# Performance work log

Measured on AMD Instinct MI355X. Metric: run time of the kernel, lower is better.

The kernel has to match this reference:

```python
import jax, jax.numpy as jnp
import numpy as np

B, S = 256, 200
VOCAB, E, H, OUT = 1002, 512, 512, 500
USERS, SKILLS = 50000, 500
PAD = 0


def setup_inputs() -> dict:
    key = jax.random.key(0)
    ks = jax.random.split(key, 16)
    s = 1.0 / np.sqrt(H)
    inp = {
        'input': jax.random.randint(ks[0], (B, S), 0, VOCAB),
        'target_id': jax.random.randint(ks[1], (B, 1), 0, OUT),
        'user_id_sequence': jax.random.randint(ks[2], (B, S), 0, USERS),
        'skill_sequence': jax.random.randint(ks[3], (B, S), 0, SKILLS),
        'attempt_sequence': jax.random.randint(ks[4], (B, S), 0, 100),
        # embeddings (padding_idx=0 -> zero row, as in torch)
        'enc_emb': (jax.random.normal(ks[5], (VOCAB, E)) * 0.02).at[PAD].set(0.0),
        'user_emb': (jax.random.normal(ks[6], (USERS, SKILLS)) * 0.02).at[PAD].set(0.0),
        'skill_emb': (jax.random.normal(ks[7], (SKILLS, SKILLS)) * 0.02).at[PAD].set(0.0),
        # MF.linear1: 2*skill_num -> hidden_dim
        'mf_W': jax.random.normal(ks[8], (H, 2 * SKILLS)) * 0.02,
        'mf_b': jnp.zeros((H,)),
        # LSTMCell params (torch gate order: i, f, g, o)
        'W_ih': jax.random.uniform(ks[9], (4 * H, E), minval=-s, maxval=s),
        'W_hh': jax.random.uniform(ks[10], (4 * H, H), minval=-s, maxval=s),
        'b_ih': jax.random.uniform(ks[11], (4 * H,), minval=-s, maxval=s),
        'b_hh': jax.random.uniform(ks[12], (4 * H,), minval=-s, maxval=s),
        # decoder: hidden -> output_dim
        'dec_W': jax.random.normal(ks[13], (OUT, H)) * 0.02,
        'dec_b': jnp.zeros((OUT,)),
    }
    return inp


def reference(input, target_id, user_id_sequence, skill_sequence, attempt_sequence,
              enc_emb, user_emb, skill_emb, mf_W, mf_b,
              W_ih, W_hh, b_ih, b_hh, dec_W, dec_b):
    # encoder embedding: (B, S, E)
    x = enc_emb[input]
    # MF branch: concat user/skill embeddings -> linear -> (B, S, H)
    ev = jnp.concatenate([user_emb[user_id_sequence], skill_emb[skill_sequence]], axis=-1)
    ext = jnp.einsum('bsf,hf->bsh', ev, mf_W) + mf_b

    def step(carry, ts):
        ht, ct = carry
        xt, et = ts  # (B, E), (B, H)
        ht = ht * jax.nn.sigmoid(et)  # custom per-step gating
        gates = xt @ W_ih.T + b_ih + ht @ W_hh.T + b_hh  # (B, 4H)
        i, f, g, o = jnp.split(gates, 4, axis=-1)
        ct = jax.nn.sigmoid(f) * ct + jax.nn.sigmoid(i) * jnp.tanh(g)
        ht = jax.nn.sigmoid(o) * jnp.tanh(ct)
        return (ht, ct), None

    h0 = jnp.zeros((B, H), dtype=x.dtype)
    (ht, _), _ = jax.lax.scan(step, (h0, h0),
                              (x.transpose(1, 0, 2), ext.transpose(1, 0, 2)))
    out = ht @ dec_W.T + dec_b  # (B, OUT)
    out = jnp.take_along_axis(out, target_id, axis=-1)  # (B, 1)
    return jax.nn.sigmoid(out)
```

## Files before the change

### kernel.cpp

```cpp
#include <hip/hip_runtime.h>
#include <stdint.h>

typedef __bf16 bf16x8 __attribute__((ext_vector_type(8)));
typedef float f32x4 __attribute__((ext_vector_type(4)));

#define MFMA16(a, b, c) __builtin_amdgcn_mfma_f32_16x16x32_bf16((a), (b), (c), 0, 0, 0)

__device__ __forceinline__ float sigf(float x) { return 1.f / (1.f + __expf(-x)); }
__device__ __forceinline__ float tanhfast(float x) { return 1.f - 2.f / (__expf(2.f * x) + 1.f); }
__device__ __forceinline__ float bf2f(uint16_t u) {
  union { float f; uint32_t i; } v; v.i = ((uint32_t)u) << 16; return v.f;
}
__device__ __forceinline__ uint16_t f2bf(float f) {
  union { float f; uint32_t i; } v; v.f = f;
  return (uint16_t)((v.i + 0x7FFFu + ((v.i >> 16) & 1u)) >> 16);
}
__device__ __forceinline__ bf16x8 cvt8(const float* __restrict__ p) {
  f32x4 a = *(const f32x4*)p;
  f32x4 b = *(const f32x4*)(p + 4);
  bf16x8 r;
  r[0] = (__bf16)a[0]; r[1] = (__bf16)a[1]; r[2] = (__bf16)a[2]; r[3] = (__bf16)a[3];
  r[4] = (__bf16)b[0]; r[5] = (__bf16)b[1]; r[6] = (__bf16)b[2]; r[7] = (__bf16)b[3];
  return r;
}

__global__ __launch_bounds__(256) void k_prep(
    const float* __restrict__ mf_W, uint16_t* __restrict__ mfWb) {
  const int idx = blockIdx.x * 256 + threadIdx.x;
  const int h = idx >> 10, k = idx & 1023;
  const float v = (k < 1000) ? mf_W[(size_t)h * 1000 + k] : 0.f;
  mfWb[idx] = f2bf(v);
}

__global__ __launch_bounds__(256) void k_encW(
    const float* __restrict__ enc_emb,
    const float* __restrict__ W_ih,
    const float* __restrict__ b_ih,
    const float* __restrict__ b_hh,
    uint16_t* __restrict__ encWb)
{
  const int w = threadIdx.x >> 6, l = threadIdx.x & 63;
  const int mblk = blockIdx.x & 15;
  const int nblk = blockIdx.x >> 4;
  const int kg = l >> 4;
  const int arow = mblk * 64 + w * 16 + (l & 15);
  const bool rowok = arow < 1002;

  f32x4 acc[4] = {};
  for (int kk = 0; kk < 16; ++kk) {
    const int kc = kk * 32 + kg * 8;
    bf16x8 a = {};
    if (rowok) a = cvt8(enc_emb + (size_t)arow * 512 + kc);
#pragma unroll
    for (int n = 0; n < 4; ++n) {
      const int wrow = nblk * 64 + n * 16 + (l & 15);
      bf16x8 b = cvt8(W_ih + (size_t)wrow * 512 + kc);
      acc[n] = MFMA16(a, b, acc[n]);
    }
  }
  const int orow = mblk * 64 + w * 16 + kg * 4;
#pragma unroll
  for (int n = 0; n < 4; ++n) {
    const int col = nblk * 64 + n * 16 + (l & 15);
    const float bias = b_ih[col] + b_hh[col];
#pragma unroll
    for (int j = 0; j < 4; ++j) {
      const int rrow = orow + j;
      if (rrow < 1002) encWb[(size_t)rrow * 2048 + col] = f2bf(acc[n][j] + bias);
    }
  }
}

__global__ __launch_bounds__(256, 2) void k_fused(
    const int* __restrict__ inp,
    const float* __restrict__ W_hh,
    const uint16_t* __restrict__ encWb,
    const int* __restrict__ uid, const int* __restrict__ sid,
    const float* __restrict__ user_emb,
    const float* __restrict__ skill_emb,
    const uint16_t* __restrict__ mfWb,
    const float* __restrict__ mf_b,
    uint16_t* __restrict__ ext,
    uint16_t* __restrict__ hbuf,
    float* __restrict__ hfinal,
    uint32_t* __restrict__ extCnt)
{
  __shared__ __align__(1024) char ldsbuf[65536];

  const int tid = threadIdx.x;
  const int w = tid >> 6, l = tid & 63, kg = l >> 4;

  if (blockIdx.x >= 256) {
    char* As = ldsbuf;
    const int bx = blockIdx.x - 256;
    const int s  = bx >> 2;
    const int bq = bx & 3;

    const int srow = tid >> 2;
    const int q = tid & 3;
    const int m = (bq * 64 + srow) * 200 + s;
    const float* up = user_emb + (size_t)uid[m] * 500;
    const float* sp = skill_emb + (size_t)sid[m] * 500;

    f32x4 acc[4][8] = {};

#pragma unroll
    for (int ks = 0; ks < 2; ++ks) {
      if (ks) __syncthreads();
#pragma unroll
      for (int j = 0; j < 16; ++j) {
        const int e0 = ks * 512 + q * 128 + j * 8;
        bf16x8 av = {};
        if (e0 + 8 <= 500) {
          av = cvt8(up + e0);
        } else if (e0 == 496) {
          f32x4 a4 = *(const f32x4*)(up + 496);
          f32x4 b4 = *(const f32x4*)sp;
          av[0] = (__bf16)a4[0]; av[1] = (__bf16)a4[1]; av[2] = (__bf16)a4[2]; av[3] = (__bf16)a4[3];
          av[4] = (__bf16)b4[0]; av[5] = (__bf16)b4[1]; av[6] = (__bf16)b4[2]; av[7] = (__bf16)b4[3];
        } else if (e0 + 8 <= 1000) {
          av = cvt8(sp + (e0 - 500));
        }
        const int kb = (q * 128 + j * 8) * 2;
        *(bf16x8*)(As + srow * 1024 + (kb ^ ((srow & 7) << 4))) = av;
      }
      __syncthreads();

      for (int kk = 0; kk < 16; ++kk) {
        bf16x8 a[4];
#pragma unroll
        for (int rf = 0; rf < 4; ++rf) {
          const int row = rf * 16 + (l & 15);
          a[rf] = *(const bf16x8*)(As + row * 1024 +
                                   ((kk * 64 + kg * 16) ^ ((row & 7) << 4)));
        }
#pragma unroll
        for (int n = 0; n < 8; ++n) {
          const int col = w * 128 + n * 16 + (l & 15);
          bf16x8 b = *(const bf16x8*)(mfWb + (size_t)col * 1024 + ks * 512 + kk * 32 + kg * 8);
#pragma unroll
          for (int rf = 0; rf < 4; ++rf)
            acc[rf][n] = MFMA16(a[rf], b, acc[rf][n]);
        }
      }
    }

#pragma unroll
    for (int rf = 0; rf < 4; ++rf)
#pragma unroll
      for (int n = 0; n < 8; ++n) {
        const int col = w * 128 + n * 16 + (l & 15);
        const float bias = mf_b[col];
#pragma unroll
        for (int j = 0; j < 4; ++j) {
          const int bl = rf * 16 + kg * 4 + j;
          const size_t grow = (size_t)(bq * 64 + bl) * 200 + s;
          ext[grow * 512 + col] = f2bf(acc[rf][n][j] + bias);
        }
      }
    asm volatile("s_waitcnt vmcnt(0)" ::: "memory");
    __syncthreads();
    if (tid == 0) {
      asm volatile("buffer_wbl2 sc1\n\ts_waitcnt vmcnt(0)" ::: "memory");
      __hip_atomic_fetch_add(extCnt + s * 16, 1u, __ATOMIC_RELAXED, __HIP_MEMORY_SCOPE_AGENT);
    }
    return;
  }

  uint16_t* htgS        = (uint16_t*)ldsbuf;
  float (*gbuf)[16][32] = (float(*)[16][32])(ldsbuf + 16384);
  float (*ctS)[32]      = (float(*)[32])(ldsbuf + 24576);
  int (*inpS)[200]      = (int(*)[200])(ldsbuf + 26624);

  const int c = blockIdx.x & 15;
  const int r = blockIdx.x >> 4;
  const int row0 = r * 16;

  bf16x8 wfrag[16][2];
#pragma unroll
  for (int kk = 0; kk < 16; ++kk) {
#pragma unroll
    for (int n = 0; n < 2; ++n) {
      const int wrow = w * 512 + c * 32 + n * 16 + (l & 15);
      wfrag[kk][n] = cvt8(W_hh + (size_t)wrow * 512 + kk * 32 + kg * 8);
    }
  }
  for (int e = tid; e < 512; e += 256) ctS[e >> 5][e & 31] = 0.f;
  for (int e = tid; e < 2048; e += 256) ((uint64_t*)htgS)[e] = 0ull;
  for (int e = tid; e < 16 * 200; e += 256)
    inpS[e / 200][e % 200] = inp[(row0 + e / 200) * 200 + (e % 200)];

  const int grow_ = l >> 2;
  const int gch = l & 3;
  const int urr = tid >> 4;
  const int uh2 = (tid & 15) << 1;
  const int ub = row0 + urr;

  __syncthreads();

  f32x4 acc[2];
#pragma unroll
  for (int n = 0; n < 2; ++n)
#pragma unroll
    for (int j = 0; j < 4; ++j) {
      const int col = w * 512 + c * 32 + n * 16 + (l & 15);
      acc[n][j] = bf2f(encWb[(size_t)inpS[kg * 4 + j][0] * 2048 + col]);
    }
  while (__hip_atomic_load(extCnt + 16, __ATOMIC_RELAXED, __HIP_MEMORY_SCOPE_AGENT) < 4u)
    __builtin_amdgcn_s_sleep(1);
  uint32_t ep = __hip_atomic_load(
      (const uint32_t*)(ext + (size_t)ub * 200 * 512 + 512 + c * 32 + uh2),
      __ATOMIC_RELAXED, __HIP_MEMORY_SCOPE_AGENT);

  for (int t = 0; t < 200; ++t) {
    if (t > 0) {
      const uint32_t tag = (uint32_t)((t >> 1) & 3);
      const uint64_t pat64 = ((uint64_t)((tag & 1u) | ((tag >> 1) << 16))) * 0x0000000100000001ull;
      const uint16_t* hb = hbuf + (size_t)(t & 1) * (256 * 512);
      const uint64_t* sp[4];
      uint64_t v[4][2];
#pragma unroll
      for (int p = 0; p < 4; ++p) {
        sp[p] = (const uint64_t*)(hb + (size_t)(row0 + grow_) * 512 + (w * 4 + p) * 32 + gch * 8);
        v[p][0] = __hip_atomic_load(sp[p],     __ATOMIC_RELAXED, __HIP_MEMORY_SCOPE_AGENT);
        v[p][1] = __hip_atomic_load(sp[p] + 1, __ATOMIC_RELAXED, __HIP_MEMORY_SCOPE_AGENT);
      }
#pragma unroll
      for (int p = 0; p < 4; ++p) {
        while ((v[p][0] & 0x0001000100010001ull) != pat64 ||
               (v[p][1] & 0x0001000100010001ull) != pat64) {
          __builtin_amdgcn_s_sleep(1);
          v[p][0] = __hip_atomic_load(sp[p],     __ATOMIC_RELAXED, __HIP_MEMORY_SCOPE_AGENT);
          v[p][1] = __hip_atomic_load(sp[p] + 1, __ATOMIC_RELAXED, __HIP_MEMORY_SCOPE_AGENT);
        }
      }
#pragma unroll
      for (int p = 0; p < 4; ++p) {
        const int prod = w * 4 + p;
        const int baddr = grow_ * 1024 + (((prod * 64) + gch * 16) ^ ((grow_ & 7) << 4));
        *(uint64_t*)((char*)htgS + baddr)     = v[p][0];
        *(uint64_t*)((char*)htgS + baddr + 8) = v[p][1];
      }
    }
    __syncthreads();

    const int ar = l & 15;
#pragma unroll
    for (int kk = 0; kk < 16; ++kk) {
      bf16x8 a = *(const bf16x8*)((char*)htgS + ar * 1024 +
                                  ((kk * 64 + kg * 16) ^ ((ar & 7) << 4)));
      acc[0] = MFMA16(a, wfrag[kk][0], acc[0]);
      acc[1] = MFMA16(a, wfrag[kk][1], acc[1]);
    }
#pragma unroll
    for (int n = 0; n < 2; ++n)
#pragma unroll
      for (int j = 0; j < 4; ++j)
        gbuf[w][kg * 4 + j][n * 16 + (l & 15)] = acc[n][j];
    __syncthreads();

    {
      float hv[2];
#pragma unroll
      for (int p = 0; p < 2; ++p) {
        const int h = uh2 + p;
        const float ig = sigf(gbuf[0][urr][h]);
        const float fg = sigf(gbuf[1][urr][h]);
        const float gg = tanhfast(gbuf[2][urr][h]);
        const float og = sigf(gbuf[3][urr][h]);
        const float cv = fg * ctS[urr][h] + ig * gg;
        ctS[urr][h] = cv;
        hv[p] = og * tanhfast(cv);
      }
      if (t < 199) {
        const float g0 = sigf(bf2f((uint16_t)(ep & 0xFFFFu)));
        const float g1 = sigf(bf2f((uint16_t)(ep >> 16)));
        const uint32_t tagn = (uint32_t)(((t + 1) >> 1) & 3);
        const uint32_t tpat = (tagn & 1u) | ((tagn >> 1) << 16);
        uint32_t pk = (uint32_t)f2bf(hv[0] * g0) | ((uint32_t)f2bf(hv[1] * g1) << 16);
        pk = (pk & ~0x00010001u) | tpat;
        uint32_t* hw = (uint32_t*)(hbuf + (size_t)((t + 1) & 1) * (256 * 512) +
                                   (size_t)ub * 512 + c * 32 + uh2);
        __hip_atomic_store(hw, pk, __ATOMIC_RELAXED, __HIP_MEMORY_SCOPE_AGENT);
      } else {
        hfinal[(size_t)ub * 512 + c * 32 + uh2]     = hv[0];
        hfinal[(size_t)ub * 512 + c * 32 + uh2 + 1] = hv[1];
      }
    }

    if (t < 199) {
      const int tn = t + 1;
#pragma unroll
      for (int n = 0; n < 2; ++n)
#pragma unroll
        for (int j = 0; j < 4; ++j) {
          const int col = w * 512 + c * 32 + n * 16 + (l & 15);
          acc[n][j] = bf2f(encWb[(size_t)inpS[kg * 4 + j][tn] * 2048 + col]);
        }
      const int te = (t + 2 < 200) ? t + 2 : 199;
      while (__hip_atomic_load(extCnt + te * 16, __ATOMIC_RELAXED, __HIP_MEMORY_SCOPE_AGENT) < 4u)
        __builtin_amdgcn_s_sleep(1);
      ep = __hip_atomic_load(
          (const uint32_t*)(ext + (size_t)ub * 200 * 512 + (size_t)te * 512 + c * 32 + uh2),
          __ATOMIC_RELAXED, __HIP_MEMORY_SCOPE_AGENT);
    }
  }
}

__global__ __launch_bounds__(256) void k_dec(
    const float* __restrict__ hfinal,
    const float* __restrict__ dec_W,
    const float* __restrict__ dec_b,
    const int* __restrict__ tgt,
    float* __restrict__ out)
{
  const int w = threadIdx.x >> 6, l = threadIdx.x & 63;
  const int b = blockIdx.x * 4 + w;
  const int t = tgt[b];
  float s = 0.f;
#pragma unroll
  for (int i = 0; i < 8; ++i) {
    const int k = l + i * 64;
    s += hfinal[(size_t)b * 512 + k] * dec_W[(size_t)t * 512 + k];
  }
#pragma unroll
  for (int m = 32; m; m >>= 1) s += __shfl_xor(s, m, 64);
  if (l == 0) out[b] = sigf(s + dec_b[t]);
}

extern "C" void kernel_launch(void* const* d_in, const int* in_sizes, int n_in,
                              void* d_out, int out_size, void* d_ws, size_t ws_size,
                              hipStream_t stream) {
  (void)in_sizes; (void)n_in; (void)out_size; (void)ws_size;
  const int*   inp       = (const int*)d_in[0];
  const int*   target_id = (const int*)d_in[1];
  const int*   uid       = (const int*)d_in[2];
  const int*   sid       = (const int*)d_in[3];
  const float* enc_emb   = (const float*)d_in[5];
  const float* user_emb  = (const float*)d_in[6];
  const float* skill_emb = (const float*)d_in[7];
  const float* mf_W      = (const float*)d_in[8];
  const float* mf_b      = (const float*)d_in[9];
  const float* W_ih      = (const float*)d_in[10];
  const float* W_hh      = (const float*)d_in[11];
  const float* b_ih      = (const float*)d_in[12];
  const float* b_hh      = (const float*)d_in[13];
  const float* dec_W     = (const float*)d_in[14];
  const float* dec_b     = (const float*)d_in[15];

  char* ws = (char*)d_ws;
  uint32_t* extCnt = (uint32_t*)(ws);
  uint16_t* hbuf   = (uint16_t*)(ws + 16384);
  float*    hfinal = (float*)   (ws + 540672);
  uint16_t* encWb  = (uint16_t*)(ws + 1064960);
  uint16_t* mfWb   = (uint16_t*)(ws + 5169152);
  uint16_t* ext    = (uint16_t*)(ws + 6217728);

  hipMemsetAsync(extCnt, 0, 12800, stream);
  hipMemsetAsync(hbuf, 0xFF, 524288, stream);

  k_prep<<<2048, 256, 0, stream>>>(mf_W, mfWb);
  k_encW<<<512,  256, 0, stream>>>(enc_emb, W_ih, b_ih, b_hh, encWb);
  k_fused<<<1056, 256, 0, stream>>>(inp, W_hh, encWb, uid, sid, user_emb, skill_emb,
                                    mfWb, mf_b, ext, hbuf, hfinal, extCnt);
  k_dec<<<64, 256, 0, stream>>>(hfinal, dec_W, dec_b, target_id, (float*)d_out);
}
```

Before: 684.7 us.

## Double block size in fused LSTM kernel, halving recurrent blocks to 128

Recurrent blocks now use 512 threads (8 waves) and each covers 64 hidden columns instead of 32, so 128 persistent blocks replace 256. Each block polls and copies fewer, larger chunks of h per step, and fewer blocks take part in the cross-block exchange. The MF producer blocks also move to 512 threads with 4 column tiles per wave. The trade is higher per-block register and LDS pressure and fewer CUs running the recurrence, with 8 waves sharing each barrier; the gate buffer is padded to 66 floats per row.

```diff
diff --git a/kernel.cpp b/kernel.cpp
--- a/kernel.cpp
+++ b/kernel.cpp
@@ -3,6 +3,7 @@
 
 typedef __bf16 bf16x8 __attribute__((ext_vector_type(8)));
 typedef float f32x4 __attribute__((ext_vector_type(4)));
+typedef float f32x2 __attribute__((ext_vector_type(2)));
 
 #define MFMA16(a, b, c) __builtin_amdgcn_mfma_f32_16x16x32_bf16((a), (b), (c), 0, 0, 0)
 
@@ -71,7 +72,7 @@
   }
 }
 
-__global__ __launch_bounds__(256, 2) void k_fused(
+__global__ __launch_bounds__(512, 2) void k_fused(
     const int* __restrict__ inp,
     const float* __restrict__ W_hh,
     const uint16_t* __restrict__ encWb,
@@ -90,26 +91,26 @@
   const int tid = threadIdx.x;
   const int w = tid >> 6, l = tid & 63, kg = l >> 4;
 
-  if (blockIdx.x >= 256) {
+  if (blockIdx.x >= 128) {
     char* As = ldsbuf;
-    const int bx = blockIdx.x - 256;
+    const int bx = blockIdx.x - 128;
     const int s  = bx >> 2;
     const int bq = bx & 3;
 
-    const int srow = tid >> 2;
-    const int q = tid & 3;
+    const int srow = tid >> 3;
+    const int q = tid & 7;
     const int m = (bq * 64 + srow) * 200 + s;
     const float* up = user_emb + (size_t)uid[m] * 500;
     const float* sp = skill_emb + (size_t)sid[m] * 500;
 
-    f32x4 acc[4][8] = {};
+    f32x4 acc[4][4] = {};
 
 #pragma unroll
     for (int ks = 0; ks < 2; ++ks) {
       if (ks) __syncthreads();
 #pragma unroll
-      for (int j = 0; j < 16; ++j) {
-        const int e0 = ks * 512 + q * 128 + j * 8;
+      for (int j = 0; j < 8; ++j) {
+        const int e0 = ks * 512 + q * 64 + j * 8;
         bf16x8 av = {};
         if (e0 + 8 <= 500) {
           av = cvt8(up + e0);
@@ -121,7 +122,7 @@
         } else if (e0 + 8 <= 1000) {
           av = cvt8(sp + (e0 - 500));
         }
-        const int kb = (q * 128 + j * 8) * 2;
+        const int kb = (q * 64 + j * 8) * 2;
         *(bf16x8*)(As + srow * 1024 + (kb ^ ((srow & 7) << 4))) = av;
       }
       __syncthreads();
@@ -135,8 +136,8 @@
                                    ((kk * 64 + kg * 16) ^ ((row & 7) << 4)));
         }
 #pragma unroll
-        for (int n = 0; n < 8; ++n) {
-          const int col = w * 128 + n * 16 + (l & 15);
+        for (int n = 0; n < 4; ++n) {
+          const int col = w * 64 + n * 16 + (l & 15);
           bf16x8 b = *(const bf16x8*)(mfWb + (size_t)col * 1024 + ks * 512 + kk * 32 + kg * 8);
 #pragma unroll
           for (int rf = 0; rf < 4; ++rf)
@@ -148,8 +149,8 @@
 #pragma unroll
     for (int rf = 0; rf < 4; ++rf)
 #pragma unroll
-      for (int n = 0; n < 8; ++n) {
-        const int col = w * 128 + n * 16 + (l & 15);
+      for (int n = 0; n < 4; ++n) {
+        const int col = w * 64 + n * 16 + (l & 15);
         const float bias = mf_b[col];
 #pragma unroll
         for (int j = 0; j < 4; ++j) {
@@ -168,32 +169,34 @@
   }
 
   uint16_t* htgS        = (uint16_t*)ldsbuf;
-  float (*gbuf)[16][32] = (float(*)[16][32])(ldsbuf + 16384);
-  float (*ctS)[32]      = (float(*)[32])(ldsbuf + 24576);
-  int (*inpS)[200]      = (int(*)[200])(ldsbuf + 26624);
-
-  const int c = blockIdx.x & 15;
-  const int r = blockIdx.x >> 4;
+  float (*gbuf)[16][66] = (float(*)[16][66])(ldsbuf + 16384);
+  float (*ctS)[64]      = (float(*)[64])(ldsbuf + 33280);
+  int (*inpS)[200]      = (int(*)[200])(ldsbuf + 37376);
+
+  const int r  = blockIdx.x >> 3;
+  const int cs = blockIdx.x & 7;
   const int row0 = r * 16;
+  const int g  = w >> 1;
+  const int hf = w & 1;
 
   bf16x8 wfrag[16][2];
 #pragma unroll
   for (int kk = 0; kk < 16; ++kk) {
 #pragma unroll
     for (int n = 0; n < 2; ++n) {
-      const int wrow = w * 512 + c * 32 + n * 16 + (l & 15);
+      const int wrow = g * 512 + cs * 64 + hf * 32 + n * 16 + (l & 15);
       wfrag[kk][n] = cvt8(W_hh + (size_t)wrow * 512 + kk * 32 + kg * 8);
     }
   }
-  for (int e = tid; e < 512; e += 256) ctS[e >> 5][e & 31] = 0.f;
-  for (int e = tid; e < 2048; e += 256) ((uint64_t*)htgS)[e] = 0ull;
-  for (int e = tid; e < 16 * 200; e += 256)
+  for (int e = tid; e < 1024; e += 512) ((float*)ctS)[e] = 0.f;
+  for (int e = tid; e < 2048; e += 512) ((uint64_t*)htgS)[e] = 0ull;
+  for (int e = tid; e < 16 * 200; e += 512)
     inpS[e / 200][e % 200] = inp[(row0 + e / 200) * 200 + (e % 200)];
 
   const int grow_ = l >> 2;
   const int gch = l & 3;
-  const int urr = tid >> 4;
-  const int uh2 = (tid & 15) << 1;
+  const int urr = tid >> 5;
+  const int uh2 = (tid & 31) << 1;
   const int ub = row0 + urr;
 
   __syncthreads();
@@ -203,13 +206,13 @@
   for (int n = 0; n < 2; ++n)
 #pragma unroll
     for (int j = 0; j < 4; ++j) {
-      const int col = w * 512 + c * 32 + n * 16 + (l & 15);
+      const int col = g * 512 + cs * 64 + hf * 32 + n * 16 + (l & 15);
       acc[n][j] = bf2f(encWb[(size_t)inpS[kg * 4 + j][0] * 2048 + col]);
     }
   while (__hip_atomic_load(extCnt + 16, __ATOMIC_RELAXED, __HIP_MEMORY_SCOPE_AGENT) < 4u)
     __builtin_amdgcn_s_sleep(1);
   uint32_t ep = __hip_atomic_load(
-      (const uint32_t*)(ext + (size_t)ub * 200 * 512 + 512 + c * 32 + uh2),
+      (const uint32_t*)(ext + (size_t)ub * 200 * 512 + 512 + cs * 64 + uh2),
       __ATOMIC_RELAXED, __HIP_MEMORY_SCOPE_AGENT);
 
   for (int t = 0; t < 200; ++t) {
@@ -217,29 +220,24 @@
       const uint32_t tag = (uint32_t)((t >> 1) & 3);
       const uint64_t pat64 = ((uint64_t)((tag & 1u) | ((tag >> 1) << 16))) * 0x0000000100000001ull;
       const uint16_t* hb = hbuf + (size_t)(t & 1) * (256 * 512);
-      const uint64_t* sp[4];
-      uint64_t v[4][2];
-#pragma unroll
-      for (int p = 0; p < 4; ++p) {
-        sp[p] = (const uint64_t*)(hb + (size_t)(row0 + grow_) * 512 + (w * 4 + p) * 32 + gch * 8);
-        v[p][0] = __hip_atomic_load(sp[p],     __ATOMIC_RELAXED, __HIP_MEMORY_SCOPE_AGENT);
-        v[p][1] = __hip_atomic_load(sp[p] + 1, __ATOMIC_RELAXED, __HIP_MEMORY_SCOPE_AGENT);
-      }
-#pragma unroll
-      for (int p = 0; p < 4; ++p) {
-        while ((v[p][0] & 0x0001000100010001ull) != pat64 ||
-               (v[p][1] & 0x0001000100010001ull) != pat64) {
-          __builtin_amdgcn_s_sleep(1);
-          v[p][0] = __hip_atomic_load(sp[p],     __ATOMIC_RELAXED, __HIP_MEMORY_SCOPE_AGENT);
-          v[p][1] = __hip_atomic_load(sp[p] + 1, __ATOMIC_RELAXED, __HIP_MEMORY_SCOPE_AGENT);
-        }
-      }
-#pragma unroll
-      for (int p = 0; p < 4; ++p) {
-        const int prod = w * 4 + p;
-        const int baddr = grow_ * 1024 + (((prod * 64) + gch * 16) ^ ((grow_ & 7) << 4));
-        *(uint64_t*)((char*)htgS + baddr)     = v[p][0];
-        *(uint64_t*)((char*)htgS + baddr + 8) = v[p][1];
+      const uint64_t* sp = (const uint64_t*)(hb + (size_t)(row0 + grow_) * 512 + w * 64 + gch * 16);
+      uint64_t v[4];
+#pragma unroll
+      for (int q = 0; q < 4; ++q)
+        v[q] = __hip_atomic_load(sp + q, __ATOMIC_RELAXED, __HIP_MEMORY_SCOPE_AGENT);
+      while ((v[0] & 0x0001000100010001ull) != pat64 ||
+             (v[1] & 0x0001000100010001ull) != pat64 ||
+             (v[2] & 0x0001000100010001ull) != pat64 ||
+             (v[3] & 0x0001000100010001ull) != pat64) {
+        __builtin_amdgcn_s_sleep(1);
+#pragma unroll
+        for (int q = 0; q < 4; ++q)
+          v[q] = __hip_atomic_load(sp + q, __ATOMIC_RELAXED, __HIP_MEMORY_SCOPE_AGENT);
+      }
+#pragma unroll
+      for (int q = 0; q < 4; ++q) {
+        const int o = w * 128 + gch * 32 + q * 8;
+        *(uint64_t*)((char*)htgS + grow_ * 1024 + (o ^ ((grow_ & 7) << 4))) = v[q];
       }
     }
     __syncthreads();
@@ -256,18 +254,23 @@
     for (int n = 0; n < 2; ++n)
 #pragma unroll
       for (int j = 0; j < 4; ++j)
-        gbuf[w][kg * 4 + j][n * 16 + (l & 15)] = acc[n][j];
+        gbuf[g][kg * 4 + j][hf * 32 + n * 16 + (l & 15)] = acc[n][j];
     __syncthreads();
 
     {
+      f32x2 sg[4];
+#pragma unroll
+      for (int gg_ = 0; gg_ < 4; ++gg_)
+        sg[gg_] = *(const f32x2*)&gbuf[gg_][urr][uh2];
+
       float hv[2];
 #pragma unroll
       for (int p = 0; p < 2; ++p) {
         const int h = uh2 + p;
-        const float ig = sigf(gbuf[0][urr][h]);
-        const float fg = sigf(gbuf[1][urr][h]);
-        const float gg = tanhfast(gbuf[2][urr][h]);
-        const float og = sigf(gbuf[3][urr][h]);
+        const float ig = sigf(sg[0][p]);
+        const float fg = sigf(sg[1][p]);
+        const float gg = tanhfast(sg[2][p]);
+        const float og = sigf(sg[3][p]);
         const float cv = fg * ctS[urr][h] + ig * gg;
         ctS[urr][h] = cv;
         hv[p] = og * tanhfast(cv);
@@ -280,11 +283,11 @@
         uint32_t pk = (uint32_t)f2bf(hv[0] * g0) | ((uint32_t)f2bf(hv[1] * g1) << 16);
         pk = (pk & ~0x00010001u) | tpat;
         uint32_t* hw = (uint32_t*)(hbuf + (size_t)((t + 1) & 1) * (256 * 512) +
-                                   (size_t)ub * 512 + c * 32 + uh2);
+                                   (size_t)ub * 512 + cs * 64 + uh2);
         __hip_atomic_store(hw, pk, __ATOMIC_RELAXED, __HIP_MEMORY_SCOPE_AGENT);
       } else {
-        hfinal[(size_t)ub * 512 + c * 32 + uh2]     = hv[0];
-        hfinal[(size_t)ub * 512 + c * 32 + uh2 + 1] = hv[1];
+        hfinal[(size_t)ub * 512 + cs * 64 + uh2]     = hv[0];
+        hfinal[(size_t)ub * 512 + cs * 64 + uh2 + 1] = hv[1];
       }
     }
 
@@ -294,14 +297,14 @@
       for (int n = 0; n < 2; ++n)
 #pragma unroll
         for (int j = 0; j < 4; ++j) {
-          const int col = w * 512 + c * 32 + n * 16 + (l & 15);
+          const int col = g * 512 + cs * 64 + hf * 32 + n * 16 + (l & 15);
           acc[n][j] = bf2f(encWb[(size_t)inpS[kg * 4 + j][tn] * 2048 + col]);
         }
       const int te = (t + 2 < 200) ? t + 2 : 199;
       while (__hip_atomic_load(extCnt + te * 16, __ATOMIC_RELAXED, __HIP_MEMORY_SCOPE_AGENT) < 4u)
         __builtin_amdgcn_s_sleep(1);
       ep = __hip_atomic_load(
-          (const uint32_t*)(ext + (size_t)ub * 200 * 512 + (size_t)te * 512 + c * 32 + uh2),
+          (const uint32_t*)(ext + (size_t)ub * 200 * 512 + (size_t)te * 512 + cs * 64 + uh2),
           __ATOMIC_RELAXED, __HIP_MEMORY_SCOPE_AGENT);
     }
   }
@@ -361,7 +364,7 @@
 
   k_prep<<<2048, 256, 0, stream>>>(mf_W, mfWb);
   k_encW<<<512,  256, 0, stream>>>(enc_emb, W_ih, b_ih, b_hh, encWb);
-  k_fused<<<1056, 256, 0, stream>>>(inp, W_hh, encWb, uid, sid, user_emb, skill_emb,
-                                    mfWb, mf_b, ext, hbuf, hfinal, extCnt);
+  k_fused<<<928, 512, 0, stream>>>(inp, W_hh, encWb, uid, sid, user_emb, skill_emb,
+                                   mfWb, mf_b, ext, hbuf, hfinal, extCnt);
   k_dec<<<64, 256, 0, stream>>>(hfinal, dec_W, dec_b, target_id, (float*)d_out);
 }
```

Measured after the change: 708.8 us (median of 2 runs). +3.5%, slower.
